# Optimization experiments

Hardware: AMD Instinct MI355X
Metric: run time of the kernel (lower is better)

## Reference

```python
import jax, jax.numpy as jnp
import numpy as np

V, E, H, B, S = 50000, 512, 1024, 256, 256


def setup_inputs() -> dict:
    key = jax.random.key(0)
    ks = jax.random.split(key, 8)
    inputs = jax.random.randint(ks[0], (B, S), 0, V)
    emb = jax.random.normal(ks[1], (V, E), dtype=jnp.float32)
    sx, sh = 1.0 / np.sqrt(E), 1.0 / np.sqrt(H)  # ~orthogonal column scale
    Wx_f = jax.random.normal(ks[2], (E, 4 * H), dtype=jnp.float32) * sx
    Wh_f = jax.random.normal(ks[3], (H, 4 * H), dtype=jnp.float32) * sh
    Wx_b = jax.random.normal(ks[4], (E, 4 * H), dtype=jnp.float32) * sx
    Wh_b = jax.random.normal(ks[5], (H, 4 * H), dtype=jnp.float32) * sh
    # gate order i, f, o, c ; forget-gate bias initialized to 1 as in the source
    bias = jnp.concatenate([jnp.zeros(H), jnp.ones(H), jnp.zeros(H), jnp.zeros(H)]).astype(jnp.float32)
    W_hq = jax.random.normal(ks[6], (H, 10), dtype=jnp.float32) * sh
    b_q = jnp.zeros(10, dtype=jnp.float32)
    return {"inputs": inputs, "emb": emb, "Wx_f": Wx_f, "Wh_f": Wh_f, "b_f": bias,
            "Wx_b": Wx_b, "Wh_b": Wh_b, "b_b": bias, "W_hq": W_hq, "b_q": b_q}


def _lstm_final_h(x_tbe, Wx, Wh, b):
    """x_tbe: [S,B,E] time-major. Returns final hidden state [B,H]."""
    h0 = jnp.zeros((x_tbe.shape[1], H), dtype=x_tbe.dtype)
    c0 = jnp.zeros_like(h0)

    def cell(carry, X):
        h, c = carry
        g = X @ Wx + h @ Wh + b          # [B, 4H] fused gate pre-activations
        i, f, o, ct = jnp.split(g, 4, axis=-1)
        c = jax.nn.sigmoid(f) * c + jax.nn.sigmoid(i) * jnp.tanh(ct)
        h = jax.nn.sigmoid(o) * jnp.tanh(c)
        return (h, c), None

    (h, _), _ = jax.lax.scan(cell, (h0, c0), x_tbe)
    return h


def reference(inputs, emb, Wx_f, Wh_f, b_f, Wx_b, Wh_b, b_b, W_hq, b_q):
    x = emb[inputs]                      # [B,S,E]
    x = jnp.transpose(x, (1, 0, 2))      # [S,B,E] time-major
    h_fwd = _lstm_final_h(x, Wx_f, Wh_f, b_f)
    h_bwd = _lstm_final_h(x[::-1], Wx_b, Wh_b, b_b)
    logits = (h_fwd + h_bwd) @ W_hq + b_q
    return jax.nn.softmax(logits, axis=1)
```

## Files before the change

kernel.cpp:

```cpp
#include <hip/hip_runtime.h>

#define S_LEN 256
#define BATCH 256
#define EDIM 512
#define HDIM 1024
#define LDS_BYTES 131072

typedef short short8 __attribute__((ext_vector_type(8)));
typedef float f32x4 __attribute__((ext_vector_type(4)));
typedef unsigned long long u64;
typedef unsigned short us;

__device__ __forceinline__ us f2bf(float f) {
  unsigned u = __float_as_uint(f);
  u = u + 0x7FFFu + ((u >> 16) & 1u);
  return (us)(u >> 16);
}
__device__ __forceinline__ float bf2f(us s) {
  return __uint_as_float(((unsigned)s) << 16);
}
__device__ __forceinline__ float sigf(float x) { return 1.0f / (1.0f + __expf(-x)); }
__device__ __forceinline__ float tanh_(float x) { return 2.0f / (1.0f + __expf(-2.0f * x)) - 1.0f; }

#define MFMA(d, a, b) d = __builtin_amdgcn_mfma_f32_16x16x32_bf16(a, b, d, 0, 0, 0)

__device__ __forceinline__ short8 load_hfrag(const us* p) {
  union { u64 d[2]; short8 v; } u;
  u.d[0] = __hip_atomic_load((const u64*)p,       __ATOMIC_RELAXED, __HIP_MEMORY_SCOPE_AGENT);
  u.d[1] = __hip_atomic_load((const u64*)(p + 4), __ATOMIC_RELAXED, __HIP_MEMORY_SCOPE_AGENT);
  return u.v;
}
__device__ __forceinline__ short8 ldf(const us* p) {
  union { uint4 d; short8 v; } u;
  u.d = *(const uint4*)p;
  return u.v;
}


__global__ void gather_embed(const int* __restrict__ inputs, const float* __restrict__ emb,
                             us* __restrict__ Xf) {
  int T = blockIdx.x * 256 + threadIdx.x;
  int kt = T & 15;
  int b  = (T >> 4) & 255;
  int s  = T >> 12;
  int vid = inputs[b * S_LEN + s];
  const float* src = emb + (size_t)vid * EDIM + kt * 32;
  int c = b & 15;
  us* ub = Xf + ((size_t)(s * 16 + kt) * 16 + (b >> 4)) * 512;
#pragma unroll
  for (int q = 0; q < 4; ++q) {
    float4 v0 = *(const float4*)(src + q * 8);
    float4 v1 = *(const float4*)(src + q * 8 + 4);
    us o[8] = { f2bf(v0.x), f2bf(v0.y), f2bf(v0.z), f2bf(v0.w),
                f2bf(v1.x), f2bf(v1.y), f2bf(v1.z), f2bf(v1.w) };
    *(uint4*)(ub + (size_t)(c + 16 * q) * 8) = *(const uint4*)o;
  }
}

__global__ void pack_w(const float* __restrict__ Wx_f, const float* __restrict__ Wh_f,
                       const float* __restrict__ Wx_b, const float* __restrict__ Wh_b,
                       us* __restrict__ Wxp, us* __restrict__ Whp) {
  int T = blockIdx.x * 256 + threadIdx.x;
  int c = T & 15;
  int q = (T >> 4) & 3;
  int t = (T >> 6) & 7;
  int r = T >> 9;
  int kit = r % 48;
  int jbd = r / 48;
  int jb  = jbd & 31;
  int dir = jbd >> 5;
  int g = t >> 1, h16 = t & 1;
  int n = g * 1024 + jb * 32 + h16 * 16 + c;
  const float* W; int k0;
  if (kit < 16) { W = dir ? Wx_b : Wx_f; k0 = kit * 32 + q * 8; }
  else          { W = dir ? Wh_b : Wh_f; k0 = (kit - 16) * 32 + q * 8; }
  us o[8];
#pragma unroll
  for (int e = 0; e < 8; ++e) o[e] = f2bf(W[(size_t)(k0 + e) * 4096 + n]);
  us* dst;
  if (kit < 16) dst = Wxp + (((size_t)(dir * 32 + jb) * 16 + kit) * 8 + t) * 512;
  else          dst = Whp + (((size_t)(dir * 32 + jb) * 32 + (kit - 16)) * 8 + t) * 512;
  *(uint4*)(dst + (size_t)(c + 16 * q) * 8) = *(const uint4*)o;
}

__global__ __launch_bounds__(512, 1) void lstm_main(
    const us* __restrict__ Xf,
    const us* __restrict__ Wxp,
    const us* __restrict__ Whp,
    const float* __restrict__ bias_f,
    const float* __restrict__ bias_b,
    us* __restrict__ Hf,
    unsigned int* __restrict__ slots)
{
  extern __shared__ __align__(16) unsigned char smem[];

  const int bx  = blockIdx.x;
  const int dir = bx & 1;
  const int mq  = (bx >> 1) & 1;
  const int J   = bx >> 2;
  const int jh  = J & 1;
  const int jt  = J >> 1;

  const int tid  = threadIdx.x;
  const int wave = tid >> 6;
  const int lane = tid & 63;
  const int c    = lane & 15;
  const int q    = lane >> 4;
  const int lofs = lane * 8;

  {
    const uint4* W4 = (const uint4*)Whp;
    for (int i = tid; i < 8192; i += 512) {
      int within = i & 63;
      int g  = (i >> 6) & 3;
      int hk = i >> 8;
      size_t src = ((((size_t)(dir * 32 + jt) * 32 + hk) * 8) + (g * 2 + jh)) * 64 + within;
      *(uint4*)(smem + (size_t)i * 16) = W4[src];
    }
  }
  const float* bias = dir ? bias_b : bias_f;
  const int j = J * 16 + c;
  float bg[4];
#pragma unroll
  for (int g = 0; g < 4; ++g) bg[g] = bias[g * HDIM + j];
  __syncthreads();

  unsigned int* grp_slots = slots + (dir * 2 + mq) * (64 * 16);
  unsigned int* my_slot   = grp_slots + J * 16;

  const int bt0 = mq * 8 + wave;
  const us* xu_base = Xf + (size_t)bt0 * 512 + lofs;
  const us* wxu = Wxp + ((size_t)(dir * 32 + jt) * 16) * 8 * 512 + (size_t)jh * 512 + lofs;
  const unsigned char* lbbase = smem + (size_t)lane * 16;

  float c_reg[4] = {0.f, 0.f, 0.f, 0.f};

  for (int s = 0; s < S_LEN; ++s) {
    const int sx = dir ? (S_LEN - 1 - s) : s;
    const int p  = s & 1;

    f32x4 acc[4];
#pragma unroll
    for (int g = 0; g < 4; ++g)
      acc[g] = (f32x4){bg[g], bg[g], bg[g], bg[g]};

    {
      const us* xu = xu_base + (size_t)sx * (16 * 16 * 512);
#pragma unroll 4
      for (int k = 0; k < 16; ++k) {
        short8 a0 = ldf(xu + (size_t)k * 8192);
        const us* wb = wxu + (size_t)k * 4096;
        short8 b0 = ldf(wb);
        short8 b1 = ldf(wb + 1024);
        short8 b2 = ldf(wb + 2048);
        short8 b3 = ldf(wb + 3072);
        MFMA(acc[0], a0, b0); MFMA(acc[1], a0, b1);
        MFMA(acc[2], a0, b2); MFMA(acc[3], a0, b3);
      }
    }

    if (s > 0) {
      if (tid < 64) {
        const unsigned int* sl = grp_slots + tid * 16;
        for (;;) {
          unsigned v = __hip_atomic_load(sl, __ATOMIC_RELAXED, __HIP_MEMORY_SCOPE_AGENT);
          if (!__any(v < (unsigned)s)) break;
          __builtin_amdgcn_s_sleep(1);
        }
      }
      __syncthreads();
      asm volatile("" ::: "memory");
    }

    {
      const us* hu = Hf + (((size_t)(p * 2 + dir) * 32) * 16 + bt0) * 512 + lofs;
      short8 pa[4];
#pragma unroll
      for (int i = 0; i < 4; ++i) pa[i] = load_hfrag(hu + (size_t)i * 8192);
#pragma unroll 4
      for (int k = 0; k < 28; ++k) {
        short8 a0 = pa[k & 3];
        pa[k & 3] = load_hfrag(hu + (size_t)(k + 4) * 8192);
        const unsigned char* lb = lbbase + (size_t)k * 4096;
        short8 b0 = *(const short8*)(lb);
        short8 b1 = *(const short8*)(lb + 1024);
        short8 b2 = *(const short8*)(lb + 2048);
        short8 b3 = *(const short8*)(lb + 3072);
        MFMA(acc[0], a0, b0); MFMA(acc[1], a0, b1);
        MFMA(acc[2], a0, b2); MFMA(acc[3], a0, b3);
      }
#pragma unroll
      for (int k = 28; k < 32; ++k) {
        short8 a0 = pa[k & 3];
        const unsigned char* lb = lbbase + (size_t)k * 4096;
        short8 b0 = *(const short8*)(lb);
        short8 b1 = *(const short8*)(lb + 1024);
        short8 b2 = *(const short8*)(lb + 2048);
        short8 b3 = *(const short8*)(lb + 3072);
        MFMA(acc[0], a0, b0); MFMA(acc[1], a0, b1);
        MFMA(acc[2], a0, b2); MFMA(acc[3], a0, b3);
      }
    }

    {
      const int q2 = jh * 2 + (c >> 3);
      const int e2 = c & 7;
      const size_t ob = ((size_t)(((p ^ 1) * 2 + dir) * 32 + jt) * 16 + bt0) * 512;
      us* hd = Hf + ob + (size_t)(16 * q2) * 8 + e2;
#pragma unroll
      for (int rg = 0; rg < 4; ++rg) {
        float gi = acc[0][rg], gf = acc[1][rg];
        float go = acc[2][rg], gc = acc[3][rg];
        float cn = sigf(gf) * c_reg[rg] + sigf(gi) * tanh_(gc);
        c_reg[rg] = cn;
        __hip_atomic_store(hd + (size_t)(q * 4 + rg) * 8, f2bf(sigf(go) * tanh_(cn)),
                           __ATOMIC_RELAXED, __HIP_MEMORY_SCOPE_AGENT);
      }
    }
    asm volatile("s_waitcnt vmcnt(0)" ::: "memory");
    __syncthreads();
    if (tid == 0)
      __hip_atomic_store(my_slot, (unsigned)(s + 1), __ATOMIC_RELAXED, __HIP_MEMORY_SCOPE_AGENT);
  }
}

__global__ void final_softmax(const us* __restrict__ Hf,
                              const float* __restrict__ Whq,
                              const float* __restrict__ bq,
                              float* __restrict__ out) {
  __shared__ float red[4][10];
  const int b = blockIdx.x;
  const int tid = threadIdx.x;
  float acc[10];
#pragma unroll
  for (int qq = 0; qq < 10; ++qq) acc[qq] = 0.f;
#pragma unroll
  for (int u = 0; u < 4; ++u) {
    int j = tid * 4 + u;
    int kt = j >> 5, q2 = (j & 31) >> 3, e = j & 7;
    size_t idx = (((size_t)kt * 16 + (b >> 4)) * 512) + ((size_t)((b & 15) + 16 * q2)) * 8 + e;
    float xv = bf2f(Hf[idx]) + bf2f(Hf[(size_t)32 * 16 * 512 + idx]);
#pragma unroll
    for (int qq = 0; qq < 10; ++qq) acc[qq] += xv * Whq[j * 10 + qq];
  }
#pragma unroll
  for (int qq = 0; qq < 10; ++qq)
#pragma unroll
    for (int off = 32; off; off >>= 1) acc[qq] += __shfl_down(acc[qq], off, 64);
  if ((tid & 63) == 0)
#pragma unroll
    for (int qq = 0; qq < 10; ++qq) red[tid >> 6][qq] = acc[qq];
  __syncthreads();
  if (tid == 0) {
    float t[10];
#pragma unroll
    for (int qq = 0; qq < 10; ++qq)
      t[qq] = red[0][qq] + red[1][qq] + red[2][qq] + red[3][qq] + bq[qq];
    float mx = t[0];
#pragma unroll
    for (int qq = 1; qq < 10; ++qq) mx = fmaxf(mx, t[qq]);
    float sum = 0.f;
#pragma unroll
    for (int qq = 0; qq < 10; ++qq) { t[qq] = __expf(t[qq] - mx); sum += t[qq]; }
    float inv = 1.0f / sum;
#pragma unroll
    for (int qq = 0; qq < 10; ++qq) out[b * 10 + qq] = t[qq] * inv;
  }
}

extern "C" void kernel_launch(void* const* d_in, const int* in_sizes, int n_in,
                              void* d_out, int out_size, void* d_ws, size_t ws_size,
                              hipStream_t stream) {
  const int*   inputs = (const int*)d_in[0];
  const float* emb    = (const float*)d_in[1];
  const float* Wx_f   = (const float*)d_in[2];
  const float* Wh_f   = (const float*)d_in[3];
  const float* b_f    = (const float*)d_in[4];
  const float* Wx_b   = (const float*)d_in[5];
  const float* Wh_b   = (const float*)d_in[6];
  const float* b_b    = (const float*)d_in[7];
  const float* W_hq   = (const float*)d_in[8];
  const float* b_q    = (const float*)d_in[9];
  float* out = (float*)d_out;

  char* ws = (char*)d_ws;
  us* Xf  = (us*)ws;
  us* Wxp = (us*)(ws + (64ull << 20));
  us* Whp = (us*)(ws + (72ull << 20));
  us* Hf  = (us*)(ws + (88ull << 20));
  unsigned int* slt = (unsigned int*)(ws + (90ull << 20));

  hipMemsetAsync(Hf, 0, (size_t)2 * 2 * 32 * 16 * 512 * sizeof(us), stream);
  hipMemsetAsync(slt, 0, 4 * 64 * 16 * sizeof(unsigned int), stream);

  gather_embed<<<4096, 256, 0, stream>>>(inputs, emb, Xf);
  pack_w<<<6144, 256, 0, stream>>>(Wx_f, Wh_f, Wx_b, Wh_b, Wxp, Whp);

  hipFuncSetAttribute((const void*)lstm_main,
                      hipFuncAttributeMaxDynamicSharedMemorySize, LDS_BYTES);

  const us* xf_p = Xf;
  const us* wxp_p = Wxp;
  const us* whp_p = Whp;
  const float* bf_p = b_f;
  const float* bb_p = b_b;
  us* hf_p = Hf;
  unsigned int* slt_p = slt;
  void* kargs[] = { (void*)&xf_p, (void*)&wxp_p, (void*)&whp_p, (void*)&bf_p,
                    (void*)&bb_p, (void*)&hf_p, (void*)&slt_p };
  hipLaunchCooperativeKernel((void*)lstm_main, dim3(256), dim3(512), kargs, LDS_BYTES, stream);

  final_softmax<<<256, 256, 0, stream>>>(Hf, W_hq, b_q, out);
}
```

Measured before the change: 4.714 ms.

## Use per-wave flag rings and packed 64-bit h stores instead of block barriers

Replaces the per-block step barrier (one polling wave plus __syncthreads, one flag per block) with per-wave flags. Each wave publishes its own step counter and waits only on the 64 producer waves that write its batch tile, so waves no longer stall on the slowest wave in their block. The hidden-state output is packed through lane shuffles into two 64-bit atomic stores per 8-element group, replacing many 16-bit atomic stores. This cuts barrier latency and store count in the sequential recurrence, but adds shuffle work and relies on per-wave memory ordering being correct.

After: 4.586 ms. 1.03x faster.

```diff
diff --git a/kernel.cpp b/kernel.cpp
--- a/kernel.cpp
+++ b/kernel.cpp
@@ -106,6 +106,8 @@
   const int lane = tid & 63;
   const int c    = lane & 15;
   const int q    = lane >> 4;
+  const int e    = c & 7;
+  const int ch   = c >> 3;
   const int lofs = lane * 8;
 
   {
@@ -125,8 +127,8 @@
   for (int g = 0; g < 4; ++g) bg[g] = bias[g * HDIM + j];
   __syncthreads();
 
-  unsigned int* grp_slots = slots + (dir * 2 + mq) * (64 * 16);
-  unsigned int* my_slot   = grp_slots + J * 16;
+  unsigned int* ring    = slots + (((dir * 2 + mq) * 8 + wave) * 64);
+  unsigned int* my_slot = ring + J;
 
   const int bt0 = mq * 8 + wave;
   const us* xu_base = Xf + (size_t)bt0 * 512 + lofs;
@@ -160,15 +162,12 @@
     }
 
     if (s > 0) {
-      if (tid < 64) {
-        const unsigned int* sl = grp_slots + tid * 16;
-        for (;;) {
-          unsigned v = __hip_atomic_load(sl, __ATOMIC_RELAXED, __HIP_MEMORY_SCOPE_AGENT);
-          if (!__any(v < (unsigned)s)) break;
-          __builtin_amdgcn_s_sleep(1);
-        }
-      }
-      __syncthreads();
+      const unsigned int* sl = ring + lane;
+      for (;;) {
+        unsigned v = __hip_atomic_load(sl, __ATOMIC_RELAXED, __HIP_MEMORY_SCOPE_AGENT);
+        if (!__any(v < (unsigned)s)) break;
+        __builtin_amdgcn_s_sleep(1);
+      }
       asm volatile("" ::: "memory");
     }
 
@@ -203,23 +202,34 @@
     }
 
     {
-      const int q2 = jh * 2 + (c >> 3);
-      const int e2 = c & 7;
       const size_t ob = ((size_t)(((p ^ 1) * 2 + dir) * 32 + jt) * 16 + bt0) * 512;
-      us* hd = Hf + ob + (size_t)(16 * q2) * 8 + e2;
+      us* hb = Hf + ob;
 #pragma unroll
       for (int rg = 0; rg < 4; ++rg) {
         float gi = acc[0][rg], gf = acc[1][rg];
         float go = acc[2][rg], gc = acc[3][rg];
         float cn = sigf(gf) * c_reg[rg] + sigf(gi) * tanh_(gc);
         c_reg[rg] = cn;
-        __hip_atomic_store(hd + (size_t)(q * 4 + rg) * 8, f2bf(sigf(go) * tanh_(cn)),
-                           __ATOMIC_RELAXED, __HIP_MEMORY_SCOPE_AGENT);
+        unsigned a = (unsigned)f2bf(sigf(go) * tanh_(cn));
+        unsigned p1 = __shfl_xor(a, 1, 64);
+        unsigned d  = (e & 1) ? ((p1 & 0xffffu) | (a << 16))
+                              : ((a  & 0xffffu) | (p1 << 16));
+        unsigned o2  = __shfl_xor(d, 2, 64);
+        unsigned lo2 = (e & 2) ? o2 : d;
+        unsigned hi2 = (e & 2) ? d  : o2;
+        unsigned ol = __shfl_xor(lo2, 4, 64);
+        unsigned oh = __shfl_xor(hi2, 4, 64);
+        u64 w0 = (e & 4) ? (((u64)oh  << 32) | ol ) : (((u64)hi2 << 32) | lo2);
+        u64 w1 = (e & 4) ? (((u64)hi2 << 32) | lo2) : (((u64)oh  << 32) | ol );
+        if (e == 0) {
+          u64* dst = (u64*)(hb + (size_t)((q * 4 + rg) + 16 * (jh * 2 + ch)) * 8);
+          __hip_atomic_store(dst,     w0, __ATOMIC_RELAXED, __HIP_MEMORY_SCOPE_AGENT);
+          __hip_atomic_store(dst + 1, w1, __ATOMIC_RELAXED, __HIP_MEMORY_SCOPE_AGENT);
+        }
       }
     }
     asm volatile("s_waitcnt vmcnt(0)" ::: "memory");
-    __syncthreads();
-    if (tid == 0)
+    if (lane == 0)
       __hip_atomic_store(my_slot, (unsigned)(s + 1), __ATOMIC_RELAXED, __HIP_MEMORY_SCOPE_AGENT);
   }
 }
@@ -291,7 +301,7 @@
   unsigned int* slt = (unsigned int*)(ws + (90ull << 20));
 
   hipMemsetAsync(Hf, 0, (size_t)2 * 2 * 32 * 16 * 512 * sizeof(us), stream);
-  hipMemsetAsync(slt, 0, 4 * 64 * 16 * sizeof(unsigned int), stream);
+  hipMemsetAsync(slt, 0, 4 * 8 * 64 * sizeof(unsigned int), stream);
 
   gather_embed<<<4096, 256, 0, stream>>>(inputs, emb, Xf);
   pack_w<<<6144, 256, 0, stream>>>(Wx_f, Wh_f, Wx_b, Wh_b, Wxp, Whp);
```
